# Kernel optimization log

Measured on AMD Instinct MI355X. Metric: run time of the kernel, lower is better.

The kernel has to match this reference:

```python
import jax, jax.numpy as jnp
import numpy as np

D_MODEL = 1024
NUM_HEADS = 16
HEAD_DIM = D_MODEL // NUM_HEADS
THETA = 10000.0
B, S = 1, 2048


def setup_inputs() -> dict:
    key = jax.random.key(0)
    ks = jax.random.split(key, 7)
    sc = 0.02
    return {
        "query": jax.random.normal(ks[0], (B, S, D_MODEL), jnp.float32),
        "key": jax.random.normal(ks[1], (B, S, D_MODEL), jnp.float32),
        "value": jax.random.normal(ks[2], (B, S, D_MODEL), jnp.float32),
        "qkv_w": jax.random.normal(ks[3], (3 * D_MODEL, D_MODEL), jnp.float32) * sc,
        "qkv_b": jax.random.normal(ks[4], (3 * D_MODEL,), jnp.float32) * sc,
        "out_w": jax.random.normal(ks[5], (D_MODEL, D_MODEL), jnp.float32) * sc,
        "out_b": jax.random.normal(ks[6], (D_MODEL,), jnp.float32) * sc,
    }


def _rope_cos_sin(seq_len, head_dim, dtype):
    # freqs_for='lang': inv_freq = theta^(-2i/d), i = 0..d/2-1
    inv_freq = 1.0 / (THETA ** (jnp.arange(0, head_dim, 2, dtype=jnp.float32) / head_dim))
    t = jnp.arange(seq_len, dtype=jnp.float32)
    freqs = jnp.outer(t, inv_freq)                      # [S, d/2]
    emb = jnp.concatenate([freqs, freqs], axis=-1)      # [S, d] (non-interleaved)
    return jnp.cos(emb).astype(dtype), jnp.sin(emb).astype(dtype)


def _rotate_half(x):
    half = x.shape[-1] // 2
    return jnp.concatenate([-x[..., half:], x[..., :half]], axis=-1)


def reference(query, key, value, qkv_w, qkv_b, out_w, out_b):
    # NOTE: module computes q,k,v all from `query` (key/value args unused).
    b, s, d = query.shape
    qkv = query @ qkv_w.T + qkv_b                       # [B,S,3D]
    qkv = qkv.reshape(b, s, 3, NUM_HEADS, HEAD_DIM)
    qkv = jnp.transpose(qkv, (2, 0, 3, 1, 4))           # [3,B,H,S,hd]
    q, k, v = qkv[0], qkv[1], qkv[2]

    cos, sin = _rope_cos_sin(s, HEAD_DIM, query.dtype)  # [S,hd]
    q = q * cos + _rotate_half(q) * sin
    k = k * cos + _rotate_half(k) * sin

    scale = 1.0 / np.sqrt(HEAD_DIM)
    scores = jnp.einsum('bhqd,bhkd->bhqk', q, k) * scale
    attn = jax.nn.softmax(scores, axis=-1)
    ctx = jnp.einsum('bhqk,bhkd->bhqd', attn, v)        # [B,H,S,hd]
    ctx = jnp.transpose(ctx, (0, 2, 1, 3)).reshape(b, s, d)
    return ctx @ out_w.T + out_b
```

## Files before the change

kernel.cpp:

```cpp
#include <hip/hip_runtime.h>
#include <math.h>
#include <stdint.h>

#define SEQ 2048
#define DM  1024
#define NH  16
#define HD  64
#define TRI 3072
#define NSPLIT 4

typedef _Float16 half8 __attribute__((ext_vector_type(8)));
typedef _Float16 half4 __attribute__((ext_vector_type(4)));
typedef __fp16 fp16x2 __attribute__((ext_vector_type(2)));
typedef float f32x4 __attribute__((ext_vector_type(4)));

#define GLOAD_LDS16(g, l)                                       \
  __builtin_amdgcn_global_load_lds(                             \
      (__attribute__((address_space(1))) void*)(g),             \
      (__attribute__((address_space(3))) void*)(l), 16, 0, 0)

#define QSCALE 0.18033688011112042f

__global__ __launch_bounds__(256)
void cvt3(const float* __restrict__ s1, const float* __restrict__ s2,
          const float* __restrict__ s3, _Float16* __restrict__ d1,
          _Float16* __restrict__ d2, _Float16* __restrict__ d3,
          float2* __restrict__ tab, int n1, int n2) {
  int b = blockIdx.x;
  if (b >= 6144) {
    int i = (b - 6144) * 256 + threadIdx.x;
    int s = i >> 5, d = i & 31;
    float inv = exp2f((float)d * -0.4152410118609203f);
    float ang = (float)s * inv;
    float sn, cs;
    sincosf(ang, &sn, &cs);
    tab[i] = make_float2(cs, sn);
    return;
  }
  int i = (b * 256 + threadIdx.x) * 4;
  const float* s; _Float16* d;
  if (i < n1)            { s = s1; d = d1; }
  else if (i < n1 + n2)  { s = s2; d = d2; i -= n1; }
  else                   { s = s3; d = d3; i -= n1 + n2; }
  float4 v = *(const float4*)(s + i);
  union { _Float16 h[4]; uint2 u; } pk;
  pk.h[0] = (_Float16)v.x; pk.h[1] = (_Float16)v.y;
  pk.h[2] = (_Float16)v.z; pk.h[3] = (_Float16)v.w;
  *(uint2*)(d + i) = pk.u;
}

__global__ __launch_bounds__(256)
void gemm_qkv(const _Float16* __restrict__ A, const _Float16* __restrict__ B,
              const float* __restrict__ bias, const float2* __restrict__ tab,
              _Float16* __restrict__ Qo, _Float16* __restrict__ Ko,
              _Float16* __restrict__ Vo) {
  constexpr int K = DM;
  __shared__ _Float16 As[2][64 * 32];
  __shared__ _Float16 Bs[2][128 * 32];

  const int t = threadIdx.x, lane = t & 63, wv = t >> 6;
  const int l15 = lane & 15, l4 = lane >> 4;
  const int wr = wv >> 1, wc = wv & 1;
  const int bm = blockIdx.y * 64, bn = blockIdx.x * 128;

  auto stage = [&](int buf, int k0) {
    {
      int c = t;
      GLOAD_LDS16(A + (size_t)(bm + (c >> 2)) * K + k0 + (c & 3) * 8,
                  (char*)&As[buf][wv * 512]);
    }
    #pragma unroll
    for (int i = 0; i < 2; ++i) {
      int c = t + i * 256;
      GLOAD_LDS16(B + (size_t)(bn + (c >> 2)) * K + k0 + (c & 3) * 8,
                  (char*)&Bs[buf][(i * 256 + wv * 64) * 8]);
    }
  };

  f32x4 acc[2][4] = {};
  stage(0, 0);
  __syncthreads();

  const int nk = K / 32;
  for (int s = 0; s < nk; ++s) {
    int cur = s & 1;
    if (s + 1 < nk) stage(cur ^ 1, (s + 1) * 32);
    half8 af[2], bf[4];
    #pragma unroll
    for (int mf = 0; mf < 2; ++mf)
      af[mf] = *(const half8*)&As[cur][(wr * 32 + mf * 16 + l15) * 32 + l4 * 8];
    #pragma unroll
    for (int nf = 0; nf < 4; ++nf)
      bf[nf] = *(const half8*)&Bs[cur][(wc * 64 + nf * 16 + l15) * 32 + l4 * 8];
    __builtin_amdgcn_s_setprio(1);
    #pragma unroll
    for (int mf = 0; mf < 2; ++mf)
      #pragma unroll
      for (int nf = 0; nf < 4; ++nf)
        acc[mf][nf] = __builtin_amdgcn_mfma_f32_16x16x32_f16(
            af[mf], bf[nf], acc[mf][nf], 0, 0, 0);
    __builtin_amdgcn_s_setprio(0);
    __syncthreads();
  }

  const int sec = bn >> 10;
  float bv[4];
  #pragma unroll
  for (int nf = 0; nf < 4; ++nf) bv[nf] = bias[bn + wc * 64 + nf * 16 + l15];

  if (sec == 0) {
    #pragma unroll
    for (int mf = 0; mf < 2; ++mf)
      #pragma unroll
      for (int r = 0; r < 4; ++r) {
        int row = bm + wr * 32 + mf * 16 + l4 * 4 + r;
        float v0 = acc[mf][0][r] + bv[0];
        float v1 = acc[mf][1][r] + bv[1];
        float v2 = acc[mf][2][r] + bv[2];
        float v3 = acc[mf][3][r] + bv[3];
        float2 cs0 = tab[row * 32 + l15];
        float2 cs1 = tab[row * 32 + 16 + l15];
        float a0 = (v0 * cs0.x - v2 * cs0.y) * QSCALE;
        float a2 = (v2 * cs0.x + v0 * cs0.y) * QSCALE;
        float a1 = (v1 * cs1.x - v3 * cs1.y) * QSCALE;
        float a3 = (v3 * cs1.x + v1 * cs1.y) * QSCALE;
        _Float16* cr = Qo + (size_t)row * DM + bn + wc * 64 + l15;
        cr[0]  = (_Float16)a0; cr[16] = (_Float16)a1;
        cr[32] = (_Float16)a2; cr[48] = (_Float16)a3;
      }
  } else if (sec == 1) {
    const int hh = ((bn - 1024) >> 6) + wc;
    const int e = l15 & 7, hi = l15 >> 3;
    #pragma unroll
    for (int mf = 0; mf < 2; ++mf)
      #pragma unroll
      for (int r = 0; r < 4; ++r) {
        int row = bm + wr * 32 + mf * 16 + l4 * 4 + r;
        float v0 = acc[mf][0][r] + bv[0];
        float v1 = acc[mf][1][r] + bv[1];
        float v2 = acc[mf][2][r] + bv[2];
        float v3 = acc[mf][3][r] + bv[3];
        float2 cs0 = tab[row * 32 + l15];
        float2 cs1 = tab[row * 32 + 16 + l15];
        float a0 = v0 * cs0.x - v2 * cs0.y;
        float a2 = v2 * cs0.x + v0 * cs0.y;
        float a1 = v1 * cs1.x - v3 * cs1.y;
        float a3 = v3 * cs1.x + v1 * cs1.y;
        int kk = row & 63, kseg = row >> 6, ks7 = kk & 7;
        size_t base = ((size_t)(hh * 32 + kseg) * 64 + kk) * 64;
        Ko[base + (((0 + hi) ^ ks7) * 8) + e] = (_Float16)a0;
        Ko[base + (((2 + hi) ^ ks7) * 8) + e] = (_Float16)a1;
        Ko[base + (((4 + hi) ^ ks7) * 8) + e] = (_Float16)a2;
        Ko[base + (((6 + hi) ^ ks7) * 8) + e] = (_Float16)a3;
      }
  } else {
    const int hh = ((bn - 2048) >> 6) + wc;
    #pragma unroll
    for (int mf = 0; mf < 2; ++mf) {
      int row0 = bm + wr * 32 + mf * 16 + l4 * 4;
      int kk0 = row0 & 63, kseg = row0 >> 6;
      #pragma unroll
      for (int nf = 0; nf < 4; ++nf) {
        int d = nf * 16 + l15;
        union { _Float16 hh4[4]; uint2 u; } pk;
        #pragma unroll
        for (int r = 0; r < 4; ++r)
          pk.hh4[r] = (_Float16)(acc[mf][nf][r] + bv[nf]);
        size_t off = ((size_t)(hh * 32 + kseg) * 64 + d) * 64 +
                     (((kk0 >> 3) ^ (d & 7)) * 8) + (kk0 & 7);
        *(uint2*)(Vo + off) = pk.u;
      }
    }
  }
}

__global__ __launch_bounds__(256)
void gemm_out(const _Float16* __restrict__ A, const _Float16* __restrict__ B,
              const float* __restrict__ bias, float* __restrict__ C) {
  constexpr int K = DM, N = DM;
  __shared__ _Float16 As[2][64 * 32];
  __shared__ _Float16 Bs[2][128 * 32];

  const int t = threadIdx.x, lane = t & 63, wv = t >> 6;
  const int l15 = lane & 15, l4 = lane >> 4;
  const int wr = wv >> 1, wc = wv & 1;
  const int bm = blockIdx.y * 64, bn = blockIdx.x * 128;

  auto stage = [&](int buf, int k0) {
    {
      int c = t;
      GLOAD_LDS16(A + (size_t)(bm + (c >> 2)) * K + k0 + (c & 3) * 8,
                  (char*)&As[buf][wv * 512]);
    }
    #pragma unroll
    for (int i = 0; i < 2; ++i) {
      int c = t + i * 256;
      GLOAD_LDS16(B + (size_t)(bn + (c >> 2)) * K + k0 + (c & 3) * 8,
                  (char*)&Bs[buf][(i * 256 + wv * 64) * 8]);
    }
  };

  f32x4 acc[2][4] = {};
  stage(0, 0);
  __syncthreads();

  const int nk = K / 32;
  for (int s = 0; s < nk; ++s) {
    int cur = s & 1;
    if (s + 1 < nk) stage(cur ^ 1, (s + 1) * 32);
    half8 af[2], bf[4];
    #pragma unroll
    for (int mf = 0; mf < 2; ++mf)
      af[mf] = *(const half8*)&As[cur][(wr * 32 + mf * 16 + l15) * 32 + l4 * 8];
    #pragma unroll
    for (int nf = 0; nf < 4; ++nf)
      bf[nf] = *(const half8*)&Bs[cur][(wc * 64 + nf * 16 + l15) * 32 + l4 * 8];
    __builtin_amdgcn_s_setprio(1);
    #pragma unroll
    for (int mf = 0; mf < 2; ++mf)
      #pragma unroll
      for (int nf = 0; nf < 4; ++nf)
        acc[mf][nf] = __builtin_amdgcn_mfma_f32_16x16x32_f16(
            af[mf], bf[nf], acc[mf][nf], 0, 0, 0);
    __builtin_amdgcn_s_setprio(0);
    __syncthreads();
  }

  float bv[4];
  #pragma unroll
  for (int nf = 0; nf < 4; ++nf) bv[nf] = bias[bn + wc * 64 + nf * 16 + l15];
  #pragma unroll
  for (int mf = 0; mf < 2; ++mf)
    #pragma unroll
    for (int r = 0; r < 4; ++r) {
      int row = bm + wr * 32 + mf * 16 + l4 * 4 + r;
      float* cr = C + (size_t)row * N + bn + wc * 64 + l15;
      cr[0]  = acc[mf][0][r] + bv[0];
      cr[16] = acc[mf][1][r] + bv[1];
      cr[32] = acc[mf][2][r] + bv[2];
      cr[48] = acc[mf][3][r] + bv[3];
    }
}

__global__ __launch_bounds__(256)
void attn_f16(const _Float16* __restrict__ Qg, const _Float16* __restrict__ Kg,
              const _Float16* __restrict__ Vg, _Float16* __restrict__ poA,
              _Float16* __restrict__ po3, float* __restrict__ pl) {
  __shared__ _Float16 Kl[2][64 * 64];
  __shared__ _Float16 Vt[2][64 * 64];

  const int t = threadIdx.x, lane = t & 63, wv = t >> 6;
  const int l15 = lane & 15, l4 = lane >> 4;
  const int bid = blockIdx.x;
  const int c = bid & 63, qb = bid >> 6;
  const int h = c & 15, z = c >> 4;
  const int q0 = qb * 128;
  const int seg0 = z * (SEQ / NSPLIT / 64);

  const _Float16* Qp = Qg + h * HD;
  const _Float16* Kbase = Kg + (size_t)h * 32 * 4096;
  const _Float16* Vbase = Vg + (size_t)h * 32 * 4096;

  half8 qf[2][2];
  #pragma unroll
  for (int qk = 0; qk < 2; ++qk) {
    const _Float16* qrow = Qp + (size_t)(q0 + wv * 32 + qk * 16 + l15) * DM;
    qf[qk][0] = *(const half8*)(qrow + l4 * 8);
    qf[qk][1] = *(const half8*)(qrow + 32 + l4 * 8);
  }

  auto issueKV = [&](int buf, int seg) {
    const _Float16* ks = Kbase + (size_t)seg * 4096;
    const _Float16* vs = Vbase + (size_t)seg * 4096;
    GLOAD_LDS16(ks + (size_t)t * 8,         (char*)&Kl[buf][(wv * 64) * 8]);
    GLOAD_LDS16(ks + (size_t)(t + 256) * 8, (char*)&Kl[buf][(256 + wv * 64) * 8]);
    GLOAD_LDS16(vs + (size_t)t * 8,         (char*)&Vt[buf][(wv * 64) * 8]);
    GLOAD_LDS16(vs + (size_t)(t + 256) * 8, (char*)&Vt[buf][(256 + wv * 64) * 8]);
  };

  f32x4 lacc[2] = {};
  f32x4 o[2][4] = {};

  issueKV(0, seg0);

  const int NT = SEQ / NSPLIT / 64;
  #pragma unroll 2
  for (int tt = 0; tt < NT; ++tt) {
    const int cur = tt & 1;
    asm volatile("s_waitcnt vmcnt(0)" ::: "memory");
    __builtin_amdgcn_s_barrier();
    __builtin_amdgcn_sched_barrier(0);
    if (tt + 1 < NT) issueKV(cur ^ 1, seg0 + tt + 1);

    f32x4 sT[2][4] = {};
    __builtin_amdgcn_s_setprio(1);
    #pragma unroll
    for (int ds = 0; ds < 2; ++ds)
      #pragma unroll
      for (int mf = 0; mf < 4; ++mf) {
        int r = mf * 16 + l15;
        int cb = ds * 4 + l4;
        half8 kf = *(const half8*)(&Kl[cur][r * 64 + ((cb ^ (r & 7)) * 8)]);
        sT[0][mf] = __builtin_amdgcn_mfma_f32_16x16x32_f16(kf, qf[0][ds], sT[0][mf], 0, 0, 0);
        sT[1][mf] = __builtin_amdgcn_mfma_f32_16x16x32_f16(kf, qf[1][ds], sT[1][mf], 0, 0, 0);
      }
    __builtin_amdgcn_s_setprio(0);

    half4 pA[2][4];
    #pragma unroll
    for (int qk = 0; qk < 2; ++qk)
      #pragma unroll
      for (int mf = 0; mf < 4; ++mf) {
        f32x4 p;
        #pragma unroll
        for (int r = 0; r < 4; ++r) p[r] = exp2f(sT[qk][mf][r]);
        lacc[qk] += p;
        union { fp16x2 h2[2]; half4 a; } pu;
        pu.h2[0] = __builtin_amdgcn_cvt_pkrtz(p[0], p[1]);
        pu.h2[1] = __builtin_amdgcn_cvt_pkrtz(p[2], p[3]);
        pA[qk][mf] = pu.a;
      }

    __builtin_amdgcn_s_setprio(1);
    #pragma unroll
    for (int mf = 0; mf < 4; ++mf) {
      int cc = ((mf * 2 + (l4 >> 1)) ^ (l15 & 7)) * 16 + (l4 & 1) * 8;
      #pragma unroll
      for (int nf = 0; nf < 4; ++nf) {
        half4 vb = *(const half4*)((char*)Vt[cur] + (nf * 16 + l15) * 128 + cc);
        o[0][nf] = __builtin_amdgcn_mfma_f32_16x16x16f16(pA[0][mf], vb, o[0][nf], 0, 0, 0);
        o[1][nf] = __builtin_amdgcn_mfma_f32_16x16x16f16(pA[1][mf], vb, o[1][nf], 0, 0, 0);
      }
    }
    __builtin_amdgcn_s_setprio(0);
  }

  _Float16* pz = (z < 3) ? (poA + (size_t)z * SEQ * DM) : po3;
  #pragma unroll
  for (int qk = 0; qk < 2; ++qk) {
    float lv = (lacc[qk][0] + lacc[qk][1]) + (lacc[qk][2] + lacc[qk][3]);
    lv += __shfl_xor(lv, 16);
    lv += __shfl_xor(lv, 32);
    #pragma unroll
    for (int nf = 0; nf < 4; ++nf)
      #pragma unroll
      for (int r = 0; r < 4; ++r) {
        int row = q0 + wv * 32 + qk * 16 + l4 * 4 + r;
        int col = h * HD + nf * 16 + l15;
        pz[(size_t)row * DM + col] = (_Float16)o[qk][nf][r];
      }
    if (l4 == 0) {
      int q = q0 + wv * 32 + qk * 16 + l15;
      pl[(z * NH + h) * SEQ + q] = lv;
    }
  }
}

__global__ __launch_bounds__(256)
void merge4(const _Float16* __restrict__ poA, const _Float16* __restrict__ po3,
            const float* __restrict__ pl, _Float16* __restrict__ ctx) {
  int e = (blockIdx.x * 256 + threadIdx.x) * 8;
  int s = e >> 10, h = (e & 1023) >> 6;
  int idx = h * SEQ + s;
  float L = pl[idx] + pl[NH * SEQ + idx] + pl[2 * NH * SEQ + idx] +
            pl[3 * NH * SEQ + idx];
  float inv = 1.0f / L;
  half8 a = *(const half8*)(poA + e);
  half8 b = *(const half8*)(poA + (size_t)SEQ * DM + e);
  half8 cc = *(const half8*)(poA + 2 * (size_t)SEQ * DM + e);
  half8 d = *(const half8*)(po3 + e);
  half8 o;
  #pragma unroll
  for (int j = 0; j < 8; ++j)
    o[j] = (_Float16)((((float)a[j] + (float)b[j]) +
                       ((float)cc[j] + (float)d[j])) * inv);
  *(half8*)(ctx + e) = o;
}

extern "C" void kernel_launch(void* const* d_in, const int* in_sizes, int n_in,
                              void* d_out, int out_size, void* d_ws, size_t ws_size,
                              hipStream_t stream) {
  const float* query = (const float*)d_in[0];
  const float* qkv_w = (const float*)d_in[3];
  const float* qkv_b = (const float*)d_in[4];
  const float* out_w = (const float*)d_in[5];
  const float* out_b = (const float*)d_in[6];
  float* out = (float*)d_out;

  char* ws = (char*)d_ws;
  _Float16* Aq   = (_Float16*)ws;
  _Float16* Wqkv = (_Float16*)(ws + (4u << 20));
  _Float16* Qb   = (_Float16*)(ws + (12u << 20));
  _Float16* Kb   = (_Float16*)(ws + (16u << 20));
  _Float16* Vb   = (_Float16*)(ws + (20u << 20));
  _Float16* ctx  = (_Float16*)(ws + (24u << 20));
  float2*   tab  = (float2*)(ws + (28u << 20));
  _Float16* Wout = (_Float16*)(ws + (28u << 20) + (512u << 10));
  float*    pl   = (float*)(ws + (30u << 20) + (512u << 10));
  _Float16* poA  = (_Float16*)ws;
  _Float16* po3  = ctx;

  cvt3<<<6400, 256, 0, stream>>>(query, qkv_w, out_w, Aq, Wqkv, Wout, tab,
                                 SEQ * DM, TRI * DM);

  gemm_qkv<<<dim3(TRI / 128, SEQ / 64), 256, 0, stream>>>(
      Aq, Wqkv, qkv_b, tab, Qb, Kb, Vb);

  attn_f16<<<(SEQ / 128) * NH * NSPLIT, 256, 0, stream>>>(
      Qb, Kb, Vb, poA, po3, pl);

  merge4<<<SEQ * DM / 8 / 256, 256, 0, stream>>>(poA, po3, pl, ctx);

  gemm_out<<<dim3(DM / 128, SEQ / 64), 256, 0, stream>>>(ctx, Wout, out_b, out);
}
```

Measured before the change: 99.34 us.

## Restructure attention to 64-query blocks with K-row permutation for 16x16x32 PV MFMA

Attention blocks now cover 64 queries (16 per wave) instead of 128, doubling the grid. The K tile rows are permuted in the QKV epilogue via a new swizzle so the score accumulators map directly onto the B operand of a 16x16x32 MFMA. The PV product can then use half8 operands and half as many MFMA instructions, and output stores become packed 8-byte writes. The trade-off is that each K/V tile loaded into LDS is reused by fewer queries, which doubles total K/V traffic.

```diff
diff --git a/kernel.cpp b/kernel.cpp
--- a/kernel.cpp
+++ b/kernel.cpp
@@ -146,12 +146,13 @@
         float a2 = v2 * cs0.x + v0 * cs0.y;
         float a1 = v1 * cs1.x - v3 * cs1.y;
         float a3 = v3 * cs1.x + v1 * cs1.y;
-        int kk = row & 63, kseg = row >> 6, ks7 = kk & 7;
+        int kk = row & 63, kseg = row >> 6;
+        int hkk = (kk & 3) | ((kk >> 1) & 4);
         size_t base = ((size_t)(hh * 32 + kseg) * 64 + kk) * 64;
-        Ko[base + (((0 + hi) ^ ks7) * 8) + e] = (_Float16)a0;
-        Ko[base + (((2 + hi) ^ ks7) * 8) + e] = (_Float16)a1;
-        Ko[base + (((4 + hi) ^ ks7) * 8) + e] = (_Float16)a2;
-        Ko[base + (((6 + hi) ^ ks7) * 8) + e] = (_Float16)a3;
+        Ko[base + (((0 + hi) ^ hkk) * 8) + e] = (_Float16)a0;
+        Ko[base + (((2 + hi) ^ hkk) * 8) + e] = (_Float16)a1;
+        Ko[base + (((4 + hi) ^ hkk) * 8) + e] = (_Float16)a2;
+        Ko[base + (((6 + hi) ^ hkk) * 8) + e] = (_Float16)a3;
       }
   } else {
     const int hh = ((bn - 2048) >> 6) + wc;
@@ -254,19 +255,18 @@
   const int bid = blockIdx.x;
   const int c = bid & 63, qb = bid >> 6;
   const int h = c & 15, z = c >> 4;
-  const int q0 = qb * 128;
+  const int q0 = qb * 64;
   const int seg0 = z * (SEQ / NSPLIT / 64);
 
   const _Float16* Qp = Qg + h * HD;
   const _Float16* Kbase = Kg + (size_t)h * 32 * 4096;
   const _Float16* Vbase = Vg + (size_t)h * 32 * 4096;
 
-  half8 qf[2][2];
-  #pragma unroll
-  for (int qk = 0; qk < 2; ++qk) {
-    const _Float16* qrow = Qp + (size_t)(q0 + wv * 32 + qk * 16 + l15) * DM;
-    qf[qk][0] = *(const half8*)(qrow + l4 * 8);
-    qf[qk][1] = *(const half8*)(qrow + 32 + l4 * 8);
+  half8 qf[2];
+  {
+    const _Float16* qrow = Qp + (size_t)(q0 + wv * 16 + l15) * DM;
+    qf[0] = *(const half8*)(qrow + l4 * 8);
+    qf[1] = *(const half8*)(qrow + 32 + l4 * 8);
   }
 
   auto issueKV = [&](int buf, int seg) {
@@ -278,8 +278,11 @@
     GLOAD_LDS16(vs + (size_t)(t + 256) * 8, (char*)&Vt[buf][(256 + wv * 64) * 8]);
   };
 
-  f32x4 lacc[2] = {};
-  f32x4 o[2][4] = {};
+  f32x4 lacc = {0.f, 0.f, 0.f, 0.f};
+  f32x4 o[4] = {};
+
+  const int hk = (l15 & 3) | (((l15 >> 2) & 1) << 2);
+  const int krow = 8 * (l15 >> 2) + (l15 & 3);
 
   issueKV(0, seg0);
 
@@ -292,67 +295,67 @@
     __builtin_amdgcn_sched_barrier(0);
     if (tt + 1 < NT) issueKV(cur ^ 1, seg0 + tt + 1);
 
-    f32x4 sT[2][4] = {};
+    f32x4 sT[4] = {};
     __builtin_amdgcn_s_setprio(1);
     #pragma unroll
     for (int ds = 0; ds < 2; ++ds)
       #pragma unroll
-      for (int mf = 0; mf < 4; ++mf) {
-        int r = mf * 16 + l15;
+      for (int m = 0; m < 4; ++m) {
+        int kappa = 32 * (m >> 1) + 4 * (m & 1) + krow;
         int cb = ds * 4 + l4;
-        half8 kf = *(const half8*)(&Kl[cur][r * 64 + ((cb ^ (r & 7)) * 8)]);
-        sT[0][mf] = __builtin_amdgcn_mfma_f32_16x16x32_f16(kf, qf[0][ds], sT[0][mf], 0, 0, 0);
-        sT[1][mf] = __builtin_amdgcn_mfma_f32_16x16x32_f16(kf, qf[1][ds], sT[1][mf], 0, 0, 0);
+        half8 kf = *(const half8*)((char*)Kl[cur] + kappa * 128 +
+                                   ((cb ^ hk) * 16));
+        sT[m] = __builtin_amdgcn_mfma_f32_16x16x32_f16(kf, qf[ds], sT[m], 0, 0, 0);
       }
     __builtin_amdgcn_s_setprio(0);
 
-    half4 pA[2][4];
-    #pragma unroll
-    for (int qk = 0; qk < 2; ++qk)
-      #pragma unroll
-      for (int mf = 0; mf < 4; ++mf) {
+    half8 pB[2];
+    #pragma unroll
+    for (int s2 = 0; s2 < 2; ++s2) {
+      union { fp16x2 h2[4]; half8 v; } pu;
+      #pragma unroll
+      for (int mh = 0; mh < 2; ++mh) {
+        int m = s2 * 2 + mh;
         f32x4 p;
         #pragma unroll
-        for (int r = 0; r < 4; ++r) p[r] = exp2f(sT[qk][mf][r]);
-        lacc[qk] += p;
-        union { fp16x2 h2[2]; half4 a; } pu;
-        pu.h2[0] = __builtin_amdgcn_cvt_pkrtz(p[0], p[1]);
-        pu.h2[1] = __builtin_amdgcn_cvt_pkrtz(p[2], p[3]);
-        pA[qk][mf] = pu.a;
-      }
+        for (int r = 0; r < 4; ++r) p[r] = exp2f(sT[m][r]);
+        lacc += p;
+        pu.h2[mh * 2 + 0] = __builtin_amdgcn_cvt_pkrtz(p[0], p[1]);
+        pu.h2[mh * 2 + 1] = __builtin_amdgcn_cvt_pkrtz(p[2], p[3]);
+      }
+      pB[s2] = pu.v;
+    }
 
     __builtin_amdgcn_s_setprio(1);
     #pragma unroll
-    for (int mf = 0; mf < 4; ++mf) {
-      int cc = ((mf * 2 + (l4 >> 1)) ^ (l15 & 7)) * 16 + (l4 & 1) * 8;
+    for (int s2 = 0; s2 < 2; ++s2)
       #pragma unroll
       for (int nf = 0; nf < 4; ++nf) {
-        half4 vb = *(const half4*)((char*)Vt[cur] + (nf * 16 + l15) * 128 + cc);
-        o[0][nf] = __builtin_amdgcn_mfma_f32_16x16x16f16(pA[0][mf], vb, o[0][nf], 0, 0, 0);
-        o[1][nf] = __builtin_amdgcn_mfma_f32_16x16x16f16(pA[1][mf], vb, o[1][nf], 0, 0, 0);
-      }
-    }
+        half8 va = *(const half8*)((char*)Vt[cur] + (nf * 16 + l15) * 128 +
+                                   (((s2 * 4 + l4) ^ (l15 & 7)) * 16));
+        o[nf] = __builtin_amdgcn_mfma_f32_16x16x32_f16(va, pB[s2], o[nf], 0, 0, 0);
+      }
     __builtin_amdgcn_s_setprio(0);
   }
 
+  float lv = (lacc[0] + lacc[1]) + (lacc[2] + lacc[3]);
+  lv += __shfl_xor(lv, 16);
+  lv += __shfl_xor(lv, 32);
   _Float16* pz = (z < 3) ? (poA + (size_t)z * SEQ * DM) : po3;
-  #pragma unroll
-  for (int qk = 0; qk < 2; ++qk) {
-    float lv = (lacc[qk][0] + lacc[qk][1]) + (lacc[qk][2] + lacc[qk][3]);
-    lv += __shfl_xor(lv, 16);
-    lv += __shfl_xor(lv, 32);
-    #pragma unroll
-    for (int nf = 0; nf < 4; ++nf)
-      #pragma unroll
-      for (int r = 0; r < 4; ++r) {
-        int row = q0 + wv * 32 + qk * 16 + l4 * 4 + r;
-        int col = h * HD + nf * 16 + l15;
-        pz[(size_t)row * DM + col] = (_Float16)o[qk][nf][r];
-      }
-    if (l4 == 0) {
-      int q = q0 + wv * 32 + qk * 16 + l15;
-      pl[(z * NH + h) * SEQ + q] = lv;
-    }
+  {
+    int row = q0 + wv * 16 + l15;
+    _Float16* pr = pz + (size_t)row * DM + h * HD + l4 * 4;
+    #pragma unroll
+    for (int nf = 0; nf < 4; ++nf) {
+      union { fp16x2 h2[2]; uint2 u; } ou;
+      ou.h2[0] = __builtin_amdgcn_cvt_pkrtz(o[nf][0], o[nf][1]);
+      ou.h2[1] = __builtin_amdgcn_cvt_pkrtz(o[nf][2], o[nf][3]);
+      *(uint2*)(pr + nf * 16) = ou.u;
+    }
+  }
+  if (l4 == 0) {
+    int q = q0 + wv * 16 + l15;
+    pl[(z * NH + h) * SEQ + q] = lv;
   }
 }
 
@@ -406,7 +409,7 @@
   gemm_qkv<<<dim3(TRI / 128, SEQ / 64), 256, 0, stream>>>(
       Aq, Wqkv, qkv_b, tab, Qb, Kb, Vb);
 
-  attn_f16<<<(SEQ / 128) * NH * NSPLIT, 256, 0, stream>>>(
+  attn_f16<<<(SEQ / 64) * NH * NSPLIT, 256, 0, stream>>>(
       Qb, Kb, Vb, poA, po3, pl);
 
   merge4<<<SEQ * DM / 8 / 256, 256, 0, stream>>>(poA, po3, pl, ctx);
```

After: 96.90 us. 2.5% less time.
